# Optimization experiments

Measured on AMD Instinct MI355X. Metric: run time of the kernel, lower is better.

Reference implementation:

```python
import jax, jax.numpy as jnp
from jax import lax
import numpy as np


def setup_inputs() -> dict:
    key = jax.random.key(0)
    encode_image = jax.random.normal(key, (32, 3, 512, 512), dtype=jnp.float32)
    return {"encode_image": encode_image, "w": 5}


def _box_blur(x, w):
    # cv2.blur with ksize (w, w): normalized box filter, BORDER_REFLECT_101 padding.
    # Implemented as a separable depthwise convolution (two 1D average passes).
    B, C, H, W = x.shape
    p = w // 2  # w is odd -> symmetric padding, matches cv2 default anchor
    xp = jnp.pad(x, ((0, 0), (0, 0), (p, p), (p, p)), mode="reflect")  # REFLECT_101
    kh = jnp.full((C, 1, w, 1), 1.0 / w, dtype=x.dtype)  # vertical pass
    kw = jnp.full((C, 1, 1, w), 1.0 / w, dtype=x.dtype)  # horizontal pass
    dn = ("NCHW", "OIHW", "NCHW")
    y = lax.conv_general_dilated(xp, kh, (1, 1), "VALID",
                                 dimension_numbers=dn, feature_group_count=C)
    y = lax.conv_general_dilated(y, kw, (1, 1), "VALID",
                                 dimension_numbers=dn, feature_group_count=C)
    return y  # (B, C, H, W)


def reference(encode_image, w):
    # Faithful to Smooth.forward: replaces noise_and_cover[0] with the box-blurred
    # image; we return the blurred tensor (the only modified element).
    return _box_blur(encode_image, w)
```

## Files before the change

### kernel.cpp

```cpp
#include <hip/hip_runtime.h>


#define WID 512
#define HEI 512
#define RPT 8
#define STRIP (4 * RPT)

__global__ __launch_bounds__(256) void smooth_box5_kernel(
    const float* __restrict__ in, float* __restrict__ out)
{
    const int tid  = threadIdx.x;
    const int lane = tid & 63;
    const int wv   = tid >> 6;
    const int c    = lane << 3;
    const int r0   = blockIdx.x * STRIP + wv * RPT;
    const long long plane = blockIdx.y;

    const float* __restrict__ ip = in  + plane * (long long)(HEI * WID);
    float*       __restrict__ op = out + plane * (long long)(HEI * WID);

    const bool Ledge = (lane == 0);
    const bool Redge = (lane == 63);

    auto loadraw = [&](int gy, float4& m0, float4& m1) {
        gy = (gy < 0) ? -gy : ((gy >= HEI) ? (2 * HEI - 2 - gy) : gy);
        const float* row = ip + gy * WID + c;
        m0 = *reinterpret_cast<const float4*>(row);
        m1 = *reinterpret_cast<const float4*>(row + 4);
    };

    auto hsum = [&](const float4 m0, const float4 m1, float h[8]) {
        float lx = __shfl_up(m1.z, 1);
        float ly = __shfl_up(m1.w, 1);
        float rx = __shfl_down(m0.x, 1);
        float ry = __shfl_down(m0.y, 1);
        if (Ledge) { lx = m0.z; ly = m0.y; }
        if (Redge) { rx = m1.z; ry = m1.y; }
        float a[12] = { lx, ly, m0.x, m0.y, m0.z, m0.w,
                        m1.x, m1.y, m1.z, m1.w, rx, ry };
        float t[11];
        #pragma unroll
        for (int j = 0; j < 11; ++j) t[j] = a[j] + a[j + 1];
        #pragma unroll
        for (int j = 0; j < 8; ++j) h[j] = t[j] + t[j + 2] + a[j + 4];
    };

    float h[5][8];
    float vs[8];
    float4 cm0, cm1, nm0, nm1;

    loadraw(r0 - 2, cm0, cm1);
    loadraw(r0 - 1, nm0, nm1);
    hsum(cm0, cm1, h[0]);
    cm0 = nm0; cm1 = nm1; loadraw(r0,     nm0, nm1);
    hsum(cm0, cm1, h[1]);
    cm0 = nm0; cm1 = nm1; loadraw(r0 + 1, nm0, nm1);
    hsum(cm0, cm1, h[2]);
    cm0 = nm0; cm1 = nm1; loadraw(r0 + 2, nm0, nm1);
    hsum(cm0, cm1, h[3]);

    #pragma unroll
    for (int j = 0; j < 8; ++j)
        vs[j] = h[0][j] + h[1][j] + h[2][j] + h[3][j];

    float* orow = op + (long long)r0 * WID + c;

    #pragma unroll
    for (int k = 0; k < RPT; ++k) {
        cm0 = nm0; cm1 = nm1;
        if (k < RPT - 1) loadraw(r0 + 3 + k, nm0, nm1);
        float hn[8];
        hsum(cm0, cm1, hn);
        #pragma unroll
        for (int j = 0; j < 8; ++j) h[(4 + k) % 5][j] = hn[j];
        float o[8];
        #pragma unroll
        for (int j = 0; j < 8; ++j) {
            vs[j] += hn[j];
            o[j] = vs[j] * 0.04f;
        }
        *reinterpret_cast<float4*>(orow)     = make_float4(o[0], o[1], o[2], o[3]);
        *reinterpret_cast<float4*>(orow + 4) = make_float4(o[4], o[5], o[6], o[7]);
        #pragma unroll
        for (int j = 0; j < 8; ++j) vs[j] -= h[k % 5][j];
        orow += WID;
    }
}

extern "C" void kernel_launch(void* const* d_in, const int* in_sizes, int n_in,
                              void* d_out, int out_size, void* d_ws, size_t ws_size,
                              hipStream_t stream) {
    const float* img = (const float*)d_in[0];
    float* out = (float*)d_out;
    const int B = 32, C = 3;
    dim3 grid(HEI / STRIP, B * C);
    dim3 block(256);
    smooth_box5_kernel<<<grid, block, 0, stream>>>(img, out);
}
```

Before: 189.5 us.

## Stage halo rows in LDS via direct global-to-LDS loads with smaller strips

```diff
diff --git a/kernel.cpp b/kernel.cpp
--- a/kernel.cpp
+++ b/kernel.cpp
@@ -3,86 +3,97 @@
 
 #define WID 512
 #define HEI 512
-#define RPT 8
-#define STRIP (4 * RPT)
+#define RPT 4
+#define STRIP 16
+#define NROW (STRIP + 4)
+
+typedef float v4f __attribute__((ext_vector_type(4)));
+typedef float v2f __attribute__((ext_vector_type(2)));
 
 __global__ __launch_bounds__(256) void smooth_box5_kernel(
     const float* __restrict__ in, float* __restrict__ out)
 {
+    __shared__ float s[NROW][WID];
+
     const int tid  = threadIdx.x;
     const int lane = tid & 63;
     const int wv   = tid >> 6;
-    const int c    = lane << 3;
-    const int r0   = blockIdx.x * STRIP + wv * RPT;
+    const int tileY = blockIdx.x * STRIP;
     const long long plane = blockIdx.y;
 
     const float* __restrict__ ip = in  + plane * (long long)(HEI * WID);
     float*       __restrict__ op = out + plane * (long long)(HEI * WID);
 
-    const bool Ledge = (lane == 0);
-    const bool Redge = (lane == 63);
+    const bool l0  = (lane == 0);
+    const bool l63 = (lane == 63);
 
-    auto loadraw = [&](int gy, float4& m0, float4& m1) {
+    #pragma unroll
+    for (int k = 0; k < 10; ++k) {
+        const int q    = wv + 4 * k;
+        const int j    = q >> 1;
+        const int half = q & 1;
+        int gy = tileY - 2 + j;
         gy = (gy < 0) ? -gy : ((gy >= HEI) ? (2 * HEI - 2 - gy) : gy);
-        const float* row = ip + gy * WID + c;
-        m0 = *reinterpret_cast<const float4*>(row);
-        m1 = *reinterpret_cast<const float4*>(row + 4);
+        const float* gp = ip + (long long)gy * WID + half * 256 + lane * 4;
+        float* lp = &s[j][half * 256];
+        __builtin_amdgcn_global_load_lds(
+            (const __attribute__((address_space(1))) void*)gp,
+            (__attribute__((address_space(3))) void*)lp,
+            16, 0, 0);
+    }
+    __syncthreads();
+
+    auto hsum = [&](int j, float h[8]) {
+        const float* row = &s[j][0];
+        const int cA = 4 * lane;
+        v4f mA = *reinterpret_cast<const v4f*>(&row[cA]);
+        v2f LA = *reinterpret_cast<const v2f*>(&row[l0 ? 0 : cA - 2]);
+        v2f RA = *reinterpret_cast<const v2f*>(&row[cA + 4]);
+        v4f mB = *reinterpret_cast<const v4f*>(&row[256 + cA]);
+        v2f LB = *reinterpret_cast<const v2f*>(&row[254 + cA]);
+        v2f RB = *reinterpret_cast<const v2f*>(&row[l63 ? 506 : 260 + cA]);
+        float e0[8] = { l0 ? mA.z : LA.x, l0 ? mA.y : LA.y,
+                        mA.x, mA.y, mA.z, mA.w, RA.x, RA.y };
+        float e1[8] = { LB.x, LB.y, mB.x, mB.y, mB.z, mB.w,
+                        l63 ? mB.z : RB.x, l63 ? mB.y : RB.y };
+        float t0[6], t1[6];
+        #pragma unroll
+        for (int m = 0; m < 6; ++m) { t0[m] = e0[m] + e0[m + 1]; t1[m] = e1[m] + e1[m + 1]; }
+        #pragma unroll
+        for (int m = 0; m < 4; ++m) {
+            h[m]     = t0[m] + t0[m + 2] + e0[m + 4];
+            h[4 + m] = t1[m] + t1[m + 2] + e1[m + 4];
+        }
     };
 
-    auto hsum = [&](const float4 m0, const float4 m1, float h[8]) {
-        float lx = __shfl_up(m1.z, 1);
-        float ly = __shfl_up(m1.w, 1);
-        float rx = __shfl_down(m0.x, 1);
-        float ry = __shfl_down(m0.y, 1);
-        if (Ledge) { lx = m0.z; ly = m0.y; }
-        if (Redge) { rx = m1.z; ry = m1.y; }
-        float a[12] = { lx, ly, m0.x, m0.y, m0.z, m0.w,
-                        m1.x, m1.y, m1.z, m1.w, rx, ry };
-        float t[11];
-        #pragma unroll
-        for (int j = 0; j < 11; ++j) t[j] = a[j] + a[j + 1];
-        #pragma unroll
-        for (int j = 0; j < 8; ++j) h[j] = t[j] + t[j + 2] + a[j + 4];
+    auto storerow = [&](float* p, const float vsum[8]) {
+        v4f o0 = { vsum[0]*0.04f, vsum[1]*0.04f, vsum[2]*0.04f, vsum[3]*0.04f };
+        v4f o1 = { vsum[4]*0.04f, vsum[5]*0.04f, vsum[6]*0.04f, vsum[7]*0.04f };
+        *reinterpret_cast<v4f*>(p + 4 * lane)       = o0;
+        *reinterpret_cast<v4f*>(p + 256 + 4 * lane) = o1;
     };
 
-    float h[5][8];
-    float vs[8];
-    float4 cm0, cm1, nm0, nm1;
+    const int jb = 4 * wv;
+    float h[4][8], hn[8], vs[8];
 
-    loadraw(r0 - 2, cm0, cm1);
-    loadraw(r0 - 1, nm0, nm1);
-    hsum(cm0, cm1, h[0]);
-    cm0 = nm0; cm1 = nm1; loadraw(r0,     nm0, nm1);
-    hsum(cm0, cm1, h[1]);
-    cm0 = nm0; cm1 = nm1; loadraw(r0 + 1, nm0, nm1);
-    hsum(cm0, cm1, h[2]);
-    cm0 = nm0; cm1 = nm1; loadraw(r0 + 2, nm0, nm1);
-    hsum(cm0, cm1, h[3]);
+    hsum(jb + 0, h[0]);
+    hsum(jb + 1, h[1]);
+    hsum(jb + 2, h[2]);
+    hsum(jb + 3, h[3]);
+    #pragma unroll
+    for (int m = 0; m < 8; ++m)
+        vs[m] = h[0][m] + h[1][m] + h[2][m] + h[3][m];
 
-    #pragma unroll
-    for (int j = 0; j < 8; ++j)
-        vs[j] = h[0][j] + h[1][j] + h[2][j] + h[3][j];
-
-    float* orow = op + (long long)r0 * WID + c;
+    float* orow = op + (long long)(tileY + 4 * wv) * WID;
 
     #pragma unroll
     for (int k = 0; k < RPT; ++k) {
-        cm0 = nm0; cm1 = nm1;
-        if (k < RPT - 1) loadraw(r0 + 3 + k, nm0, nm1);
-        float hn[8];
-        hsum(cm0, cm1, hn);
+        hsum(jb + 4 + k, hn);
         #pragma unroll
-        for (int j = 0; j < 8; ++j) h[(4 + k) % 5][j] = hn[j];
-        float o[8];
+        for (int m = 0; m < 8; ++m) vs[m] += hn[m];
+        storerow(orow, vs);
         #pragma unroll
-        for (int j = 0; j < 8; ++j) {
-            vs[j] += hn[j];
-            o[j] = vs[j] * 0.04f;
-        }
-        *reinterpret_cast<float4*>(orow)     = make_float4(o[0], o[1], o[2], o[3]);
-        *reinterpret_cast<float4*>(orow + 4) = make_float4(o[4], o[5], o[6], o[7]);
-        #pragma unroll
-        for (int j = 0; j < 8; ++j) vs[j] -= h[k % 5][j];
+        for (int m = 0; m < 8; ++m) vs[m] -= h[k][m];
         orow += WID;
     }
 }
```

Measured after the change: 177.0 us. -6.6%, faster.
